# Optimization experiments

Hardware: AMD Instinct MI355X
Metric: run time of the kernel (lower is better)

Reference implementation:

```python
import jax, jax.numpy as jnp
import numpy as np

V, E, H, ENC_D, NL = 32000, 1024, 1024, 1024, 2
N, DEC_L, ENC_L, A = 32, 64, 64, 1024


def gru_cell(x, h, W_ih, W_hh, b_ih, b_hh):
    # PyTorch GRUCell math
    gi = x @ W_ih.T + b_ih            # N x 3H
    gh = h @ W_hh.T + b_hh            # N x 3H
    i_r, i_z, i_n = jnp.split(gi, 3, axis=-1)
    h_r, h_z, h_n = jnp.split(gh, 3, axis=-1)
    r = jax.nn.sigmoid(i_r + h_r)
    z = jax.nn.sigmoid(i_z + h_z)
    n = jnp.tanh(i_n + r * h_n)
    return (1.0 - z) * n + z * h


def setup_inputs() -> dict:
    key = jax.random.key(0)
    ks = jax.random.split(key, 16)
    s = 0.05
    emb_table = jax.random.normal(ks[0], (V, E), jnp.float32) * s
    emb_table = emb_table.at[0].set(0.0)  # padding_idx = 0
    inp = {
        "input_ids": jax.random.randint(ks[1], (N, DEC_L), 0, V),
        "dec_init": jax.random.normal(ks[2], (NL, N, H), jnp.float32),
        "enc_hids": jax.random.normal(ks[3], (N, ENC_L, ENC_D), jnp.float32),
        "emb_table": emb_table,
        "W_in": jax.random.normal(ks[4], (H, E), jnp.float32) * s,
        "b_in": jnp.zeros((H,), jnp.float32),
        "W_ctx": jax.random.normal(ks[5], (H, ENC_D), jnp.float32) * s,
        "b_ctx": jnp.zeros((H,), jnp.float32),
        "W_att_dec": jax.random.normal(ks[6], (A, H), jnp.float32) * s,
        "W_att_enc": jax.random.normal(ks[7], (A, ENC_D), jnp.float32) * s,
        "v_att": jax.random.normal(ks[8], (A,), jnp.float32) * s,
        "W_ih": jax.random.normal(ks[9], (NL, 3 * H, H), jnp.float32) * s,
        "W_hh": jax.random.normal(ks[10], (NL, 3 * H, H), jnp.float32) * s,
        "b_ih": jnp.zeros((NL, 3 * H), jnp.float32),
        "b_hh": jnp.zeros((NL, 3 * H), jnp.float32),
    }
    return inp


def reference(input_ids, dec_init, enc_hids, emb_table, W_in, b_in, W_ctx, b_ctx,
              W_att_dec, W_att_enc, v_att, W_ih, W_hh, b_ih, b_hh):
    ids = input_ids[:, :-1]                      # N x T (T = dec_L - 1)
    # precompute encoder side of additive attention: N x enc_L x A
    enc_proj = jnp.einsum('nld,ad->nla', enc_hids, W_att_enc)
    n_layers = W_ih.shape[0]

    def step(h_stack, x_ids):
        h_top = h_stack[-1]                       # N x H
        emb = emb_table[x_ids]                    # N x E
        # Bahdanau additive attention: v^T tanh(Wd h + We enc)
        dec_proj = h_top @ W_att_dec.T            # N x A
        score = jnp.einsum('nla,a->nl', jnp.tanh(enc_proj + dec_proj[:, None, :]), v_att)
        att = jax.nn.softmax(score, axis=-1)      # N x enc_L
        ctx = jnp.einsum('nl,nld->nd', att, enc_hids)  # N x enc_D
        merged = emb @ W_in.T + b_in + ctx @ W_ctx.T + b_ctx  # N x H
        layer_in = merged
        hs = []
        for l in range(n_layers):
            h_new = gru_cell(layer_in, h_stack[l], W_ih[l], W_hh[l], b_ih[l], b_hh[l])
            layer_in = h_new
            hs.append(h_new)
        new_stack = jnp.stack(hs, axis=0)
        return new_stack, (layer_in, att)

    dec_prev, (hs, atts) = jax.lax.scan(step, dec_init, ids.T)  # hs: T x N x H
    dec_hids = jnp.transpose(hs, (1, 0, 2))       # N x T x H
    atts = jnp.transpose(atts, (1, 2, 0))         # N x enc_L x T
    return dec_hids, atts, dec_prev
```

## Files before the change

### kernel.cpp

```cpp
#include <hip/hip_runtime.h>
#include <cstddef>

typedef unsigned short ushort_t;
typedef __attribute__((ext_vector_type(8))) short bhalf8;
typedef __attribute__((ext_vector_type(4))) unsigned short ushort4v;
typedef __attribute__((ext_vector_type(4))) float floatx4;

#define T_STEPS 63

__device__ __forceinline__ float bf2f(unsigned short u) {
  union { unsigned int i; float f; } c; c.i = ((unsigned int)u) << 16; return c.f;
}
__device__ __forceinline__ unsigned short f2bf(float f) {
  union { float f; unsigned int i; } c; c.f = f;
  unsigned int x = c.i;
  return (unsigned short)((x + 0x7FFFu + ((x >> 16) & 1u)) >> 16);
}
__device__ __forceinline__ float tanh_f(float x) {
  float e = exp2f(x * 2.8853900817779268f);
  return 1.f - 2.f / (e + 1.f);
}
__device__ __forceinline__ float sigm_f(float x) {
  return 1.f / (1.f + exp2f(x * -1.4426950408889634f));
}

__global__ __launch_bounds__(256) void conv_k(const float* __restrict__ in,
                                              ushort_t* __restrict__ outp, int n4) {
  int g = blockIdx.x * 256 + threadIdx.x;
  if (g < n4) {
    floatx4 v = ((const floatx4*)in)[g];
    ushort4v o;
    o[0] = f2bf(v[0]); o[1] = f2bf(v[1]); o[2] = f2bf(v[2]); o[3] = f2bf(v[3]);
    ((ushort4v*)outp)[g] = o;
  }
}

__global__ __launch_bounds__(256) void bsum_k(const float* __restrict__ b_in,
    const float* __restrict__ b_ctx, const float* __restrict__ v_att,
    float* __restrict__ bsum, ushort_t* __restrict__ vattbf) {
  int i = blockIdx.x * 256 + threadIdx.x;
  if (i < 1024) {
    bsum[i] = b_in[i] + b_ctx[i];
    vattbf[i] = f2bf(v_att[i]);
  }
}

__global__ __launch_bounds__(256) void init_k(const float* __restrict__ dec_init,
    float* __restrict__ h1, float* __restrict__ h2,
    ushort_t* __restrict__ h1bf, ushort_t* __restrict__ h2bf) {
  int g = blockIdx.x * 256 + threadIdx.x;
  int l = g >> 15, idx = g & 32767;
  float f = dec_init[g];
  if (l == 0) { h1[idx] = f; h1bf[idx] = f2bf(f); }
  else        { h2[idx] = f; h2bf[idx] = f2bf(f); }
}

__global__ __launch_bounds__(256) void encp_s(const float* __restrict__ enc_hids,
    const float* __restrict__ Wae, ushort_t* __restrict__ encp) {
  int g = blockIdx.x * 256 + threadIdx.x;
  int r = g >> 10, c = g & 1023;
  const float* x = enc_hids + (size_t)r * 1024;
  const float* w = Wae + (size_t)c * 1024;
  float s = 0.f;
  for (int k = 0; k < 1024; k += 4) {
    floatx4 a = *(const floatx4*)(x + k);
    floatx4 b = *(const floatx4*)(w + k);
    s += a[0] * b[0] + a[1] * b[1] + a[2] * b[2] + a[3] * b[3];
  }
  encp[g] = f2bf(s);
}

__global__ __launch_bounds__(256) void membp_s(const int* __restrict__ ids,
    const float* __restrict__ emb_table, const float* __restrict__ W_in,
    const float* __restrict__ bsum, ushort_t* __restrict__ membp) {
  int g = blockIdx.x * 256 + threadIdx.x;
  int row = g >> 10, c = g & 1023;
  int t = row >> 5, n = row & 31;
  const float* e = emb_table + (size_t)ids[n * 64 + t] * 1024;
  const float* w = W_in + (size_t)c * 1024;
  float s = bsum[c];
  for (int k = 0; k < 1024; k += 4) {
    floatx4 a = *(const floatx4*)(e + k);
    floatx4 b = *(const floatx4*)(w + k);
    s += a[0] * b[0] + a[1] * b[1] + a[2] * b[2] + a[3] * b[3];
  }
  membp[g] = f2bf(s);
}

__global__ __launch_bounds__(256) void stage0_k(
    const ushort_t* __restrict__ h1bf, const ushort_t* __restrict__ h2bf,
    const ushort_t* __restrict__ Wad, const ushort_t* __restrict__ Whh,
    const float* __restrict__ bhh,
    float* __restrict__ dprj, float* __restrict__ gh1, float* __restrict__ gh2) {
  __shared__ __align__(16) ushort_t sXk[32 * 264];
  __shared__ __align__(16) ushort_t sBk[32 * 264];
  int b = blockIdx.x, tid = threadIdx.x;
  int wid = tid >> 6, lane = tid & 63;
  int klane = (lane >> 4) << 3;
  const ushort_t *Xs, *Wp; const float* bp; float* Co; int ldc, colbase;
  if (b < 32)       { Xs = h2bf; Wp = Wad;           bp = nullptr;     Co = dprj; ldc = 1024; colbase = b * 32; }
  else if (b < 128) { Xs = h1bf; Wp = Whh;           bp = bhh;         Co = gh1;  ldc = 3072; colbase = (b - 32) * 32; }
  else              { Xs = h2bf; Wp = Whh + 3145728; bp = bhh + 3072;  Co = gh2;  ldc = 3072; colbase = (b - 128) * 32; }
  int nt = wid & 1, mt = wid >> 1;
  floatx4 acc = {0, 0, 0, 0};
  for (int kp = 0; kp < 4; ++kp) {
    __syncthreads();
    #pragma unroll
    for (int it = 0; it < 4; ++it) {
      int v = it * 256 + tid; int row = v >> 5, vc = v & 31;
      *(bhalf8*)(&sXk[row * 264 + vc * 8]) = *(const bhalf8*)(Xs + (size_t)row * 1024 + kp * 256 + vc * 8);
      *(bhalf8*)(&sBk[row * 264 + vc * 8]) = *(const bhalf8*)(Wp + (size_t)(colbase + row) * 1024 + kp * 256 + vc * 8);
    }
    __syncthreads();
    #pragma unroll
    for (int kit = 0; kit < 8; ++kit) {
      int k = kit * 32 + klane;
      bhalf8 a  = *(const bhalf8*)(&sXk[(mt * 16 + (lane & 15)) * 264 + k]);
      bhalf8 bf = *(const bhalf8*)(&sBk[(nt * 16 + (lane & 15)) * 264 + k]);
      acc = __builtin_amdgcn_mfma_f32_16x16x32_bf16(a, bf, acc, 0, 0, 0);
    }
  }
  int colw = colbase + nt * 16 + (lane & 15);
  float bv = bp ? bp[colw] : 0.f;
  int r0 = (lane >> 4) << 2;
  #pragma unroll
  for (int i = 0; i < 4; ++i)
    Co[(size_t)(mt * 16 + r0 + i) * ldc + colw] = acc[i] + bv;
}

__global__ __launch_bounds__(256) void att_k(int t,
    const ushort_t* __restrict__ encp, const float* __restrict__ dprj,
    const ushort_t* __restrict__ vattbf, const float* __restrict__ enc_hids,
    ushort_t* __restrict__ ctxbf, float* __restrict__ out_att) {
  __shared__ float sSc[64];
  __shared__ float sAtt[64];
  int n = blockIdx.x, tid = threadIdx.x;
  int l = tid >> 2, q = tid & 3;
  const ushort_t* ep = encp + ((size_t)(n * 64 + l)) * 1024 + q * 256;
  const float*    dp = dprj + n * 1024 + q * 256;
  float p = 0.f;
  for (int it = 0; it < 32; ++it) {
    bhalf8 E = *(const bhalf8*)(ep + it * 8);
    bhalf8 V = *(const bhalf8*)(vattbf + q * 256 + it * 8);
    #pragma unroll
    for (int r = 0; r < 8; ++r)
      p += tanh_f(bf2f((unsigned short)E[r]) + dp[it * 8 + r]) * bf2f((unsigned short)V[r]);
  }
  p += __shfl_down(p, 1, 4);
  p += __shfl_down(p, 2, 4);
  if (q == 0) sSc[l] = p;
  __syncthreads();
  if (tid < 64) {
    float s = sSc[tid];
    float m = s;
    for (int off = 32; off; off >>= 1) m = fmaxf(m, __shfl_xor(m, off));
    float e = exp2f((s - m) * 1.4426950408889634f);
    float sum = e;
    for (int off = 32; off; off >>= 1) sum += __shfl_xor(sum, off);
    float a = e / sum;
    sAtt[tid] = a;
    out_att[(size_t)n * 4032 + tid * 63 + t] = a;
  }
  __syncthreads();
  const float* er = enc_hids + ((size_t)n * 64) * 1024 + tid * 4;
  float c0 = 0, c1 = 0, c2 = 0, c3 = 0;
  for (int l2 = 0; l2 < 64; ++l2) {
    floatx4 ev = *(const floatx4*)(er + (size_t)l2 * 1024);
    float a = sAtt[l2];
    c0 += a * ev[0]; c1 += a * ev[1]; c2 += a * ev[2]; c3 += a * ev[3];
  }
  ushort_t* cp = ctxbf + n * 1024 + tid * 4;
  cp[0] = f2bf(c0); cp[1] = f2bf(c1); cp[2] = f2bf(c2); cp[3] = f2bf(c3);
}

__global__ __launch_bounds__(256) void mctx_k(
    const ushort_t* __restrict__ ctxbf, const ushort_t* __restrict__ Wctx,
    const ushort_t* __restrict__ membp_t, ushort_t* __restrict__ mctx) {
  __shared__ __align__(16) ushort_t sXk[32 * 264];
  __shared__ __align__(16) ushort_t sBk[32 * 264];
  int b = blockIdx.x, tid = threadIdx.x;
  int wid = tid >> 6, lane = tid & 63;
  int klane = (lane >> 4) << 3;
  int colbase = b * 32;
  int nt = wid & 1, mt = wid >> 1;
  floatx4 acc = {0, 0, 0, 0};
  for (int kp = 0; kp < 4; ++kp) {
    __syncthreads();
    #pragma unroll
    for (int it = 0; it < 4; ++it) {
      int v = it * 256 + tid; int row = v >> 5, vc = v & 31;
      *(bhalf8*)(&sXk[row * 264 + vc * 8]) = *(const bhalf8*)(ctxbf + (size_t)row * 1024 + kp * 256 + vc * 8);
      *(bhalf8*)(&sBk[row * 264 + vc * 8]) = *(const bhalf8*)(Wctx + (size_t)(colbase + row) * 1024 + kp * 256 + vc * 8);
    }
    __syncthreads();
    #pragma unroll
    for (int kit = 0; kit < 8; ++kit) {
      int k = kit * 32 + klane;
      bhalf8 a  = *(const bhalf8*)(&sXk[(mt * 16 + (lane & 15)) * 264 + k]);
      bhalf8 bf = *(const bhalf8*)(&sBk[(nt * 16 + (lane & 15)) * 264 + k]);
      acc = __builtin_amdgcn_mfma_f32_16x16x32_bf16(a, bf, acc, 0, 0, 0);
    }
  }
  int colw = colbase + nt * 16 + (lane & 15);
  int r0 = (lane >> 4) << 2;
  #pragma unroll
  for (int i = 0; i < 4; ++i) {
    int row = mt * 16 + r0 + i;
    mctx[(size_t)row * 1024 + colw] = f2bf(acc[i] + bf2f(membp_t[(size_t)row * 1024 + colw]));
  }
}

__global__ __launch_bounds__(256) void gru_k(
    const ushort_t* __restrict__ Xs, const ushort_t* __restrict__ Wg,
    const float* __restrict__ gh, const float* __restrict__ hp,
    float* __restrict__ ho, ushort_t* __restrict__ hobf,
    const float* __restrict__ add,
    float* __restrict__ outh) {
  __shared__ __align__(16) ushort_t sX16[16 * 1032];
  __shared__ __align__(16) float sRed[2304];
  int b = blockIdx.x, tid = threadIdx.x;
  int wid = tid >> 6, lane = tid & 63;
  int mh = b & 1, g = b >> 1, j0 = g * 16;
  #pragma unroll
  for (int it = 0; it < 8; ++it) {
    int v = it * 256 + tid; int row = v >> 7, vc = v & 127;
    *(bhalf8*)(&sX16[row * 1032 + vc * 8]) = *(const bhalf8*)(Xs + (size_t)(mh * 16 + row) * 1024 + vc * 8);
  }
  __syncthreads();
  floatx4 a0 = {0,0,0,0}, a1 = {0,0,0,0}, a2 = {0,0,0,0};
  int klane = (lane >> 4) << 3;
  const ushort_t* Wr = Wg + (size_t)(j0 + (lane & 15)) * 1024;
  for (int kit = 0; kit < 8; ++kit) {
    int k = wid * 256 + kit * 32 + klane;
    bhalf8 a = *(const bhalf8*)(&sX16[(lane & 15) * 1032 + k]);
    a0 = __builtin_amdgcn_mfma_f32_16x16x32_bf16(a, *(const bhalf8*)(Wr + k), a0, 0, 0, 0);
    a1 = __builtin_amdgcn_mfma_f32_16x16x32_bf16(a, *(const bhalf8*)(Wr + 1048576 + k), a1, 0, 0, 0);
    a2 = __builtin_amdgcn_mfma_f32_16x16x32_bf16(a, *(const bhalf8*)(Wr + 2097152 + k), a2, 0, 0, 0);
  }
  if (wid) {
    ((floatx4*)sRed)[((wid - 1) * 3 + 0) * 64 + lane] = a0;
    ((floatx4*)sRed)[((wid - 1) * 3 + 1) * 64 + lane] = a1;
    ((floatx4*)sRed)[((wid - 1) * 3 + 2) * 64 + lane] = a2;
  }
  __syncthreads();
  if (wid == 0) {
    #pragma unroll
    for (int w = 0; w < 3; ++w) {
      a0 += ((floatx4*)sRed)[(w * 3 + 0) * 64 + lane];
      a1 += ((floatx4*)sRed)[(w * 3 + 1) * 64 + lane];
      a2 += ((floatx4*)sRed)[(w * 3 + 2) * 64 + lane];
    }
    int col = j0 + (lane & 15), r0 = (lane >> 4) << 2;
    #pragma unroll
    for (int i = 0; i < 4; ++i) {
      int n = mh * 16 + r0 + i;
      float ir  = a0[i] + add[col];
      float iz  = a1[i] + add[col + 1024];
      float inn = a2[i] + add[col + 2048];
      int gb = n * 3072 + col;
      float r = sigm_f(ir + gh[gb]);
      float z = sigm_f(iz + gh[gb + 1024]);
      float nn = tanh_f(inn + r * gh[gb + 2048]);
      float h = (1.f - z) * nn + z * hp[n * 1024 + col];
      ho[n * 1024 + col] = h;
      hobf[n * 1024 + col] = f2bf(h);
      if (outh) outh[(size_t)n * 64512 + col] = h;
    }
  }
}

__global__ __launch_bounds__(256) void final_k(const float* __restrict__ h1,
                                               const float* __restrict__ h2,
                                               float* __restrict__ outp) {
  int b = blockIdx.x; int l = b >> 5, n = b & 31;
  const float* src = l ? h2 : h1;
  float* dst = outp + (size_t)l * 32768 + n * 1024;
  for (int c = threadIdx.x; c < 1024; c += 256) dst[c] = src[n * 1024 + c];
}

extern "C" void kernel_launch(void* const* d_in, const int* in_sizes, int n_in,
                              void* d_out, int out_size, void* d_ws, size_t ws_size,
                              hipStream_t stream) {
  const int*   input_ids = (const int*)d_in[0];
  const float* dec_init  = (const float*)d_in[1];
  const float* enc_hids  = (const float*)d_in[2];
  const float* emb_table = (const float*)d_in[3];
  const float* W_in      = (const float*)d_in[4];
  const float* b_in      = (const float*)d_in[5];
  const float* b_ctx     = (const float*)d_in[7];
  const float* W_att_dec = (const float*)d_in[8];
  const float* W_att_enc = (const float*)d_in[9];
  const float* v_att     = (const float*)d_in[10];
  const float* W_ih      = (const float*)d_in[11];
  const float* W_hh      = (const float*)d_in[12];
  const float* b_ih      = (const float*)d_in[13];
  const float* b_hh      = (const float*)d_in[14];
  const float* W_ctx     = (const float*)d_in[6];
  (void)in_sizes; (void)n_in; (void)out_size;

  const size_t WS_NEEDED = 39133184;
  if (ws_size < WS_NEEDED) return;
  char* ws = (char*)d_ws;
  float*    h1      = (float*)   (ws + 0);
  float*    h2      = (float*)   (ws + 131072);
  ushort_t* h1bf    = (ushort_t*)(ws + 262144);
  ushort_t* h2bf    = (ushort_t*)(ws + 327680);
  ushort_t* ctxbf   = (ushort_t*)(ws + 393216);
  ushort_t* mctx    = (ushort_t*)(ws + 458752);
  float*    dprj    = (float*)   (ws + 524288);
  float*    gh1     = (float*)   (ws + 655360);
  float*    gh2     = (float*)   (ws + 1048576);
  float*    bsum    = (float*)   (ws + 1441792);
  ushort_t* vattbf  = (ushort_t*)(ws + 1445888);
  ushort_t* encp    = (ushort_t*)(ws + 1449984);
  ushort_t* membp   = (ushort_t*)(ws + 5644288);
  ushort_t* Whh_bf  = (ushort_t*)(ws + 9773056);
  ushort_t* Wih_bf  = (ushort_t*)(ws + 22355968);
  ushort_t* Wad_bf  = (ushort_t*)(ws + 34938880);
  ushort_t* Wctx_bf = (ushort_t*)(ws + 37036032);

  float* out_hid  = (float*)d_out;
  float* out_att  = out_hid + 2064384;
  float* out_prev = out_att + 129024;

  bsum_k<<<dim3(4), dim3(256), 0, stream>>>(b_in, b_ctx, v_att, bsum, vattbf);
  init_k<<<dim3(256), dim3(256), 0, stream>>>(dec_init, h1, h2, h1bf, h2bf);
  conv_k<<<dim3(6144), dim3(256), 0, stream>>>(W_hh, Whh_bf, 1572864);
  conv_k<<<dim3(6144), dim3(256), 0, stream>>>(W_ih, Wih_bf, 1572864);
  conv_k<<<dim3(1024), dim3(256), 0, stream>>>(W_att_dec, Wad_bf, 262144);
  conv_k<<<dim3(1024), dim3(256), 0, stream>>>(W_ctx, Wctx_bf, 262144);
  encp_s<<<dim3(8192), dim3(256), 0, stream>>>(enc_hids, W_att_enc, encp);
  membp_s<<<dim3(8064), dim3(256), 0, stream>>>(input_ids, emb_table, W_in, bsum, membp);

  for (int t = 0; t < T_STEPS; ++t) {
    stage0_k<<<dim3(224), dim3(256), 0, stream>>>(h1bf, h2bf, Wad_bf, Whh_bf, b_hh,
                                                  dprj, gh1, gh2);
    att_k<<<dim3(32), dim3(256), 0, stream>>>(t, encp, dprj, vattbf, enc_hids,
                                              ctxbf, out_att);
    mctx_k<<<dim3(32), dim3(256), 0, stream>>>(ctxbf, Wctx_bf, membp + (size_t)t * 32768, mctx);
    gru_k<<<dim3(128), dim3(256), 0, stream>>>(mctx, Wih_bf, gh1, h1, h1, h1bf,
                                               b_ih, (float*)nullptr);
    gru_k<<<dim3(128), dim3(256), 0, stream>>>(h1bf, Wih_bf + 3145728, gh2, h2, h2, h2bf,
                                               b_ih + 3072, out_hid + (size_t)t * 1024);
  }
  final_k<<<dim3(64), dim3(256), 0, stream>>>(h1, h2, out_prev);
}
```

Baseline: 5.831 ms.

## Fuse decoder time loop into persistent kernel with global barriers

Replaces the per-step sequence of five kernel launches with one persistent 224-block kernel. Stages inside each step are separated by atomic-counter grid barriers, and the attention-to-merge dependency uses a smaller barrier over 32 blocks. The precomputed embedding projection (membp) is removed and computed per step inside the merge GEMM from gathered embedding rows and a bf16 W_in. The layer-1 Whh GEMM for the next step now overlaps the layer-2 GRU on idle blocks. This removes launch overhead but assumes all 224 blocks are co-resident, and the spin barrier has a bail-out that could silently break ordering.

```diff
diff --git a/kernel.cpp b/kernel.cpp
--- a/kernel.cpp
+++ b/kernel.cpp
@@ -7,6 +7,7 @@
 typedef __attribute__((ext_vector_type(4))) float floatx4;
 
 #define T_STEPS 63
+#define GRID_N 224
 
 __device__ __forceinline__ float bf2f(unsigned short u) {
   union { unsigned int i; float f; } c; c.i = ((unsigned int)u) << 16; return c.f;
@@ -37,8 +38,10 @@
 
 __global__ __launch_bounds__(256) void bsum_k(const float* __restrict__ b_in,
     const float* __restrict__ b_ctx, const float* __restrict__ v_att,
-    float* __restrict__ bsum, ushort_t* __restrict__ vattbf) {
+    float* __restrict__ bsum, ushort_t* __restrict__ vattbf,
+    unsigned* __restrict__ bar) {
   int i = blockIdx.x * 256 + threadIdx.x;
+  if (i == 0) { bar[0] = 0u; bar[128] = 0u; }
   if (i < 1024) {
     bsum[i] = b_in[i] + b_ctx[i];
     vattbf[i] = f2bf(v_att[i]);
@@ -70,37 +73,12 @@
   encp[g] = f2bf(s);
 }
 
-__global__ __launch_bounds__(256) void membp_s(const int* __restrict__ ids,
-    const float* __restrict__ emb_table, const float* __restrict__ W_in,
-    const float* __restrict__ bsum, ushort_t* __restrict__ membp) {
-  int g = blockIdx.x * 256 + threadIdx.x;
-  int row = g >> 10, c = g & 1023;
-  int t = row >> 5, n = row & 31;
-  const float* e = emb_table + (size_t)ids[n * 64 + t] * 1024;
-  const float* w = W_in + (size_t)c * 1024;
-  float s = bsum[c];
-  for (int k = 0; k < 1024; k += 4) {
-    floatx4 a = *(const floatx4*)(e + k);
-    floatx4 b = *(const floatx4*)(w + k);
-    s += a[0] * b[0] + a[1] * b[1] + a[2] * b[2] + a[3] * b[3];
-  }
-  membp[g] = f2bf(s);
-}
-
-__global__ __launch_bounds__(256) void stage0_k(
-    const ushort_t* __restrict__ h1bf, const ushort_t* __restrict__ h2bf,
-    const ushort_t* __restrict__ Wad, const ushort_t* __restrict__ Whh,
-    const float* __restrict__ bhh,
-    float* __restrict__ dprj, float* __restrict__ gh1, float* __restrict__ gh2) {
-  __shared__ __align__(16) ushort_t sXk[32 * 264];
-  __shared__ __align__(16) ushort_t sBk[32 * 264];
-  int b = blockIdx.x, tid = threadIdx.x;
+__device__ __forceinline__ void tile32(const ushort_t* __restrict__ Xs,
+    const ushort_t* __restrict__ Wp, const float* __restrict__ bias,
+    float* __restrict__ Co, int ldc, int colbase,
+    ushort_t* sXk, ushort_t* sBk, int tid) {
   int wid = tid >> 6, lane = tid & 63;
   int klane = (lane >> 4) << 3;
-  const ushort_t *Xs, *Wp; const float* bp; float* Co; int ldc, colbase;
-  if (b < 32)       { Xs = h2bf; Wp = Wad;           bp = nullptr;     Co = dprj; ldc = 1024; colbase = b * 32; }
-  else if (b < 128) { Xs = h1bf; Wp = Whh;           bp = bhh;         Co = gh1;  ldc = 3072; colbase = (b - 32) * 32; }
-  else              { Xs = h2bf; Wp = Whh + 3145728; bp = bhh + 3072;  Co = gh2;  ldc = 3072; colbase = (b - 128) * 32; }
   int nt = wid & 1, mt = wid >> 1;
   floatx4 acc = {0, 0, 0, 0};
   for (int kp = 0; kp < 4; ++kp) {
@@ -121,104 +99,55 @@
     }
   }
   int colw = colbase + nt * 16 + (lane & 15);
-  float bv = bp ? bp[colw] : 0.f;
+  float bv = bias ? bias[colw] : 0.f;
   int r0 = (lane >> 4) << 2;
   #pragma unroll
   for (int i = 0; i < 4; ++i)
     Co[(size_t)(mt * 16 + r0 + i) * ldc + colw] = acc[i] + bv;
 }
 
-__global__ __launch_bounds__(256) void att_k(int t,
-    const ushort_t* __restrict__ encp, const float* __restrict__ dprj,
-    const ushort_t* __restrict__ vattbf, const float* __restrict__ enc_hids,
-    ushort_t* __restrict__ ctxbf, float* __restrict__ out_att) {
-  __shared__ float sSc[64];
-  __shared__ float sAtt[64];
-  int n = blockIdx.x, tid = threadIdx.x;
-  int l = tid >> 2, q = tid & 3;
-  const ushort_t* ep = encp + ((size_t)(n * 64 + l)) * 1024 + q * 256;
-  const float*    dp = dprj + n * 1024 + q * 256;
-  float p = 0.f;
-  for (int it = 0; it < 32; ++it) {
-    bhalf8 E = *(const bhalf8*)(ep + it * 8);
-    bhalf8 V = *(const bhalf8*)(vattbf + q * 256 + it * 8);
-    #pragma unroll
-    for (int r = 0; r < 8; ++r)
-      p += tanh_f(bf2f((unsigned short)E[r]) + dp[it * 8 + r]) * bf2f((unsigned short)V[r]);
-  }
-  p += __shfl_down(p, 1, 4);
-  p += __shfl_down(p, 2, 4);
-  if (q == 0) sSc[l] = p;
-  __syncthreads();
-  if (tid < 64) {
-    float s = sSc[tid];
-    float m = s;
-    for (int off = 32; off; off >>= 1) m = fmaxf(m, __shfl_xor(m, off));
-    float e = exp2f((s - m) * 1.4426950408889634f);
-    float sum = e;
-    for (int off = 32; off; off >>= 1) sum += __shfl_xor(sum, off);
-    float a = e / sum;
-    sAtt[tid] = a;
-    out_att[(size_t)n * 4032 + tid * 63 + t] = a;
-  }
-  __syncthreads();
-  const float* er = enc_hids + ((size_t)n * 64) * 1024 + tid * 4;
-  float c0 = 0, c1 = 0, c2 = 0, c3 = 0;
-  for (int l2 = 0; l2 < 64; ++l2) {
-    floatx4 ev = *(const floatx4*)(er + (size_t)l2 * 1024);
-    float a = sAtt[l2];
-    c0 += a * ev[0]; c1 += a * ev[1]; c2 += a * ev[2]; c3 += a * ev[3];
-  }
-  ushort_t* cp = ctxbf + n * 1024 + tid * 4;
-  cp[0] = f2bf(c0); cp[1] = f2bf(c1); cp[2] = f2bf(c2); cp[3] = f2bf(c3);
-}
-
-__global__ __launch_bounds__(256) void mctx_k(
-    const ushort_t* __restrict__ ctxbf, const ushort_t* __restrict__ Wctx,
-    const ushort_t* __restrict__ membp_t, ushort_t* __restrict__ mctx) {
+__global__ __launch_bounds__(256) void ginit_k(const ushort_t* __restrict__ h1bf,
+    const ushort_t* __restrict__ Whh, const float* __restrict__ bhh,
+    float* __restrict__ gh1) {
   __shared__ __align__(16) ushort_t sXk[32 * 264];
   __shared__ __align__(16) ushort_t sBk[32 * 264];
-  int b = blockIdx.x, tid = threadIdx.x;
-  int wid = tid >> 6, lane = tid & 63;
-  int klane = (lane >> 4) << 3;
-  int colbase = b * 32;
-  int nt = wid & 1, mt = wid >> 1;
-  floatx4 acc = {0, 0, 0, 0};
-  for (int kp = 0; kp < 4; ++kp) {
-    __syncthreads();
-    #pragma unroll
-    for (int it = 0; it < 4; ++it) {
-      int v = it * 256 + tid; int row = v >> 5, vc = v & 31;
-      *(bhalf8*)(&sXk[row * 264 + vc * 8]) = *(const bhalf8*)(ctxbf + (size_t)row * 1024 + kp * 256 + vc * 8);
-      *(bhalf8*)(&sBk[row * 264 + vc * 8]) = *(const bhalf8*)(Wctx + (size_t)(colbase + row) * 1024 + kp * 256 + vc * 8);
-    }
-    __syncthreads();
-    #pragma unroll
-    for (int kit = 0; kit < 8; ++kit) {
-      int k = kit * 32 + klane;
-      bhalf8 a  = *(const bhalf8*)(&sXk[(mt * 16 + (lane & 15)) * 264 + k]);
-      bhalf8 bf = *(const bhalf8*)(&sBk[(nt * 16 + (lane & 15)) * 264 + k]);
-      acc = __builtin_amdgcn_mfma_f32_16x16x32_bf16(a, bf, acc, 0, 0, 0);
-    }
-  }
-  int colw = colbase + nt * 16 + (lane & 15);
-  int r0 = (lane >> 4) << 2;
-  #pragma unroll
-  for (int i = 0; i < 4; ++i) {
-    int row = mt * 16 + r0 + i;
-    mctx[(size_t)row * 1024 + colw] = f2bf(acc[i] + bf2f(membp_t[(size_t)row * 1024 + colw]));
-  }
-}
-
-__global__ __launch_bounds__(256) void gru_k(
+  tile32(h1bf, Whh, bhh, gh1, 3072, blockIdx.x * 32, sXk, sBk, threadIdx.x);
+}
+
+struct PArgs {
+  const float *enc_hids, *bhh, *bih, *emb_table, *bsum;
+  const int* ids;
+  const ushort_t *Whh, *Wih, *Wad, *Wctx, *Win, *encp, *vatt;
+  float *h1, *h2, *dprj, *gh1, *gh2;
+  ushort_t *h1bf, *h2bf, *ctxbf, *mctxbf;
+  float *out_hid, *out_att, *out_prev;
+  unsigned* bar;
+};
+
+__device__ __forceinline__ void gbar_n(unsigned* bar, unsigned& ph, unsigned nblk) {
+  __syncthreads();
+  if (threadIdx.x == 0) {
+    __threadfence();
+    __hip_atomic_fetch_add(bar, 1u, __ATOMIC_RELAXED, __HIP_MEMORY_SCOPE_AGENT);
+    unsigned tgt = (++ph) * nblk;
+    unsigned spins = 0;
+    while (__hip_atomic_load(bar, __ATOMIC_RELAXED, __HIP_MEMORY_SCOPE_AGENT) < tgt) {
+      if (spins < 8)       __builtin_amdgcn_s_sleep(2);
+      else if (spins < 32) __builtin_amdgcn_s_sleep(16);
+      else                 __builtin_amdgcn_s_sleep(64);
+      if (++spins > (1u << 20)) break;
+    }
+    __threadfence();
+  }
+  __syncthreads();
+}
+
+__device__ __forceinline__ void gru_body(int b, int tid,
     const ushort_t* __restrict__ Xs, const ushort_t* __restrict__ Wg,
     const float* __restrict__ gh, const float* __restrict__ hp,
     float* __restrict__ ho, ushort_t* __restrict__ hobf,
-    const float* __restrict__ add,
-    float* __restrict__ outh) {
-  __shared__ __align__(16) ushort_t sX16[16 * 1032];
-  __shared__ __align__(16) float sRed[2304];
-  int b = blockIdx.x, tid = threadIdx.x;
+    const float* __restrict__ add, float* __restrict__ outh,
+    ushort_t* sX16, float* sRed) {
   int wid = tid >> 6, lane = tid & 63;
   int mh = b & 1, g = b >> 1, j0 = g * 16;
   #pragma unroll
@@ -269,13 +198,143 @@
   }
 }
 
-__global__ __launch_bounds__(256) void final_k(const float* __restrict__ h1,
-                                               const float* __restrict__ h2,
-                                               float* __restrict__ outp) {
-  int b = blockIdx.x; int l = b >> 5, n = b & 31;
-  const float* src = l ? h2 : h1;
-  float* dst = outp + (size_t)l * 32768 + n * 1024;
-  for (int c = threadIdx.x; c < 1024; c += 256) dst[c] = src[n * 1024 + c];
+__global__ __launch_bounds__(256) void decoder_pers(PArgs A) {
+  __shared__ __align__(16) unsigned char smemU[42240];
+  __shared__ float sSc[64];
+  __shared__ float sAtt[64];
+  __shared__ int sIds[32];
+  ushort_t* sXk  = (ushort_t*)smemU;
+  ushort_t* sBk  = (ushort_t*)(smemU + 16896);
+  ushort_t* sX16 = (ushort_t*)smemU;
+  float*    sRed = (float*)(smemU + 33024);
+
+  const int b = blockIdx.x, tid = threadIdx.x;
+  unsigned ph = 0, phm = 0;
+  unsigned* barF = A.bar;
+  unsigned* barM = A.bar + 128;
+
+  for (int t = 0; t < T_STEPS; ++t) {
+    if (b < 32)        tile32(A.h2bf, A.Wad, nullptr, A.dprj, 1024, b * 32, sXk, sBk, tid);
+    else if (b < 128)  tile32(A.h2bf, A.Whh + 3145728, A.bhh + 3072, A.gh2, 3072, (b - 32) * 32, sXk, sBk, tid);
+    gbar_n(barF, ph, GRID_N);
+
+    if (b < 32) {
+      int n = b;
+      int l = tid >> 2, q = tid & 3;
+      const ushort_t* ep = A.encp + ((size_t)(n * 64 + l)) * 1024 + q * 256;
+      const float*    dp = A.dprj + n * 1024 + q * 256;
+      float p = 0.f;
+      for (int it = 0; it < 32; ++it) {
+        bhalf8 E = *(const bhalf8*)(ep + it * 8);
+        bhalf8 V = *(const bhalf8*)(A.vatt + q * 256 + it * 8);
+        #pragma unroll
+        for (int r = 0; r < 8; ++r)
+          p += tanh_f(bf2f((unsigned short)E[r]) + dp[it * 8 + r]) * bf2f((unsigned short)V[r]);
+      }
+      p += __shfl_down(p, 1, 4);
+      p += __shfl_down(p, 2, 4);
+      if (q == 0) sSc[l] = p;
+      __syncthreads();
+      if (tid < 64) {
+        float s = sSc[tid];
+        float m = s;
+        for (int off = 32; off; off >>= 1) m = fmaxf(m, __shfl_xor(m, off));
+        float e = exp2f((s - m) * 1.4426950408889634f);
+        float sum = e;
+        for (int off = 32; off; off >>= 1) sum += __shfl_xor(sum, off);
+        float a = e / sum;
+        sAtt[tid] = a;
+        A.out_att[(size_t)n * 4032 + tid * 63 + t] = a;
+      }
+      __syncthreads();
+      const float* er = A.enc_hids + ((size_t)n * 64) * 1024 + tid * 4;
+      float c0 = 0, c1 = 0, c2 = 0, c3 = 0;
+      for (int l2 = 0; l2 < 64; ++l2) {
+        floatx4 ev = *(const floatx4*)(er + (size_t)l2 * 1024);
+        float a = sAtt[l2];
+        c0 += a * ev[0]; c1 += a * ev[1]; c2 += a * ev[2]; c3 += a * ev[3];
+      }
+      ushort_t* cp = A.ctxbf + n * 1024 + tid * 4;
+      cp[0] = f2bf(c0); cp[1] = f2bf(c1); cp[2] = f2bf(c2); cp[3] = f2bf(c3);
+
+      gbar_n(barM, phm, 32);
+
+      int colbase = b * 32;
+      if (tid < 32) sIds[tid] = A.ids[tid * 64 + t];
+      __syncthreads();
+      int wid = tid >> 6, lane = tid & 63;
+      int klane = (lane >> 4) << 3;
+      int nt = wid & 1, mt = wid >> 1;
+      floatx4 acc = {0, 0, 0, 0};
+      for (int kp = 0; kp < 4; ++kp) {
+        __syncthreads();
+        #pragma unroll
+        for (int it = 0; it < 4; ++it) {
+          int v = it * 256 + tid; int row = v >> 5, vc = v & 31;
+          *(bhalf8*)(&sXk[row * 264 + vc * 8]) = *(const bhalf8*)(A.ctxbf + (size_t)row * 1024 + kp * 256 + vc * 8);
+          *(bhalf8*)(&sBk[row * 264 + vc * 8]) = *(const bhalf8*)(A.Wctx + (size_t)(colbase + row) * 1024 + kp * 256 + vc * 8);
+        }
+        __syncthreads();
+        #pragma unroll
+        for (int kit = 0; kit < 8; ++kit) {
+          int k = kit * 32 + klane;
+          bhalf8 a  = *(const bhalf8*)(&sXk[(mt * 16 + (lane & 15)) * 264 + k]);
+          bhalf8 bf = *(const bhalf8*)(&sBk[(nt * 16 + (lane & 15)) * 264 + k]);
+          acc = __builtin_amdgcn_mfma_f32_16x16x32_bf16(a, bf, acc, 0, 0, 0);
+        }
+        __syncthreads();
+        #pragma unroll
+        for (int it = 0; it < 4; ++it) {
+          int v = it * 256 + tid; int row = v >> 5, vc = v & 31;
+          const float* epp = A.emb_table + (size_t)sIds[row] * 1024 + kp * 256 + vc * 8;
+          floatx4 f0 = *(const floatx4*)epp;
+          floatx4 f1 = *(const floatx4*)(epp + 4);
+          bhalf8 o;
+          o[0] = (short)f2bf(f0[0]); o[1] = (short)f2bf(f0[1]);
+          o[2] = (short)f2bf(f0[2]); o[3] = (short)f2bf(f0[3]);
+          o[4] = (short)f2bf(f1[0]); o[5] = (short)f2bf(f1[1]);
+          o[6] = (short)f2bf(f1[2]); o[7] = (short)f2bf(f1[3]);
+          *(bhalf8*)(&sXk[row * 264 + vc * 8]) = o;
+          *(bhalf8*)(&sBk[row * 264 + vc * 8]) = *(const bhalf8*)(A.Win + (size_t)(colbase + row) * 1024 + kp * 256 + vc * 8);
+        }
+        __syncthreads();
+        #pragma unroll
+        for (int kit = 0; kit < 8; ++kit) {
+          int k = kit * 32 + klane;
+          bhalf8 a  = *(const bhalf8*)(&sXk[(mt * 16 + (lane & 15)) * 264 + k]);
+          bhalf8 bf = *(const bhalf8*)(&sBk[(nt * 16 + (lane & 15)) * 264 + k]);
+          acc = __builtin_amdgcn_mfma_f32_16x16x32_bf16(a, bf, acc, 0, 0, 0);
+        }
+      }
+      int colw = colbase + nt * 16 + (lane & 15);
+      int r0 = (lane >> 4) << 2;
+      #pragma unroll
+      for (int i = 0; i < 4; ++i) {
+        int row = mt * 16 + r0 + i;
+        A.mctxbf[(size_t)row * 1024 + colw] = f2bf(acc[i] + A.bsum[colw]);
+      }
+    }
+    gbar_n(barF, ph, GRID_N);
+
+    if (b < 128)
+      gru_body(b, tid, A.mctxbf, A.Wih, A.gh1, A.h1, A.h1, A.h1bf,
+               A.bih, nullptr, sX16, sRed);
+    gbar_n(barF, ph, GRID_N);
+
+    if (b < 128)
+      gru_body(b, tid, A.h1bf, A.Wih + 3145728, A.gh2, A.h2, A.h2, A.h2bf,
+               A.bih + 3072, A.out_hid + (size_t)t * 1024, sX16, sRed);
+    else
+      tile32(A.h1bf, A.Whh, A.bhh, A.gh1, 3072, (b - 128) * 32, sXk, sBk, tid);
+    gbar_n(barF, ph, GRID_N);
+  }
+
+  if (b < 64) {
+    int l = b >> 5, n = b & 31;
+    const float* src = l ? A.h2 : A.h1;
+    float* dst = A.out_prev + (size_t)l * 32768 + n * 1024;
+    for (int c = tid; c < 1024; c += 256) dst[c] = src[n * 1024 + c];
+  }
 }
 
 extern "C" void kernel_launch(void* const* d_in, const int* in_sizes, int n_in,
@@ -287,6 +346,7 @@
   const float* emb_table = (const float*)d_in[3];
   const float* W_in      = (const float*)d_in[4];
   const float* b_in      = (const float*)d_in[5];
+  const float* W_ctx     = (const float*)d_in[6];
   const float* b_ctx     = (const float*)d_in[7];
   const float* W_att_dec = (const float*)d_in[8];
   const float* W_att_enc = (const float*)d_in[9];
@@ -295,10 +355,9 @@
   const float* W_hh      = (const float*)d_in[12];
   const float* b_ih      = (const float*)d_in[13];
   const float* b_hh      = (const float*)d_in[14];
-  const float* W_ctx     = (const float*)d_in[6];
   (void)in_sizes; (void)n_in; (void)out_size;
 
-  const size_t WS_NEEDED = 39133184;
+  const size_t WS_NEEDED = 37105664;
   if (ws_size < WS_NEEDED) return;
   char* ws = (char*)d_ws;
   float*    h1      = (float*)   (ws + 0);
@@ -306,42 +365,42 @@
   ushort_t* h1bf    = (ushort_t*)(ws + 262144);
   ushort_t* h2bf    = (ushort_t*)(ws + 327680);
   ushort_t* ctxbf   = (ushort_t*)(ws + 393216);
-  ushort_t* mctx    = (ushort_t*)(ws + 458752);
+  ushort_t* mctxbf  = (ushort_t*)(ws + 458752);
   float*    dprj    = (float*)   (ws + 524288);
   float*    gh1     = (float*)   (ws + 655360);
   float*    gh2     = (float*)   (ws + 1048576);
   float*    bsum    = (float*)   (ws + 1441792);
   ushort_t* vattbf  = (ushort_t*)(ws + 1445888);
-  ushort_t* encp    = (ushort_t*)(ws + 1449984);
-  ushort_t* membp   = (ushort_t*)(ws + 5644288);
-  ushort_t* Whh_bf  = (ushort_t*)(ws + 9773056);
-  ushort_t* Wih_bf  = (ushort_t*)(ws + 22355968);
-  ushort_t* Wad_bf  = (ushort_t*)(ws + 34938880);
-  ushort_t* Wctx_bf = (ushort_t*)(ws + 37036032);
+  unsigned* bar     = (unsigned*)(ws + 1449984);
+  ushort_t* encp    = (ushort_t*)(ws + 1454080);
+  ushort_t* Win_bf  = (ushort_t*)(ws + 5648384);
+  ushort_t* Wctx_bf = (ushort_t*)(ws + 7745536);
+  ushort_t* Wad_bf  = (ushort_t*)(ws + 9842688);
+  ushort_t* Whh_bf  = (ushort_t*)(ws + 11939840);
+  ushort_t* Wih_bf  = (ushort_t*)(ws + 24522752);
 
   float* out_hid  = (float*)d_out;
   float* out_att  = out_hid + 2064384;
   float* out_prev = out_att + 129024;
 
-  bsum_k<<<dim3(4), dim3(256), 0, stream>>>(b_in, b_ctx, v_att, bsum, vattbf);
+  bsum_k<<<dim3(4), dim3(256), 0, stream>>>(b_in, b_ctx, v_att, bsum, vattbf, bar);
   init_k<<<dim3(256), dim3(256), 0, stream>>>(dec_init, h1, h2, h1bf, h2bf);
   conv_k<<<dim3(6144), dim3(256), 0, stream>>>(W_hh, Whh_bf, 1572864);
   conv_k<<<dim3(6144), dim3(256), 0, stream>>>(W_ih, Wih_bf, 1572864);
   conv_k<<<dim3(1024), dim3(256), 0, stream>>>(W_att_dec, Wad_bf, 262144);
   conv_k<<<dim3(1024), dim3(256), 0, stream>>>(W_ctx, Wctx_bf, 262144);
+  conv_k<<<dim3(1024), dim3(256), 0, stream>>>(W_in, Win_bf, 262144);
   encp_s<<<dim3(8192), dim3(256), 0, stream>>>(enc_hids, W_att_enc, encp);
-  membp_s<<<dim3(8064), dim3(256), 0, stream>>>(input_ids, emb_table, W_in, bsum, membp);
-
-  for (int t = 0; t < T_STEPS; ++t) {
-    stage0_k<<<dim3(224), dim3(256), 0, stream>>>(h1bf, h2bf, Wad_bf, Whh_bf, b_hh,
-                                                  dprj, gh1, gh2);
-    att_k<<<dim3(32), dim3(256), 0, stream>>>(t, encp, dprj, vattbf, enc_hids,
-                                              ctxbf, out_att);
-    mctx_k<<<dim3(32), dim3(256), 0, stream>>>(ctxbf, Wctx_bf, membp + (size_t)t * 32768, mctx);
-    gru_k<<<dim3(128), dim3(256), 0, stream>>>(mctx, Wih_bf, gh1, h1, h1, h1bf,
-                                               b_ih, (float*)nullptr);
-    gru_k<<<dim3(128), dim3(256), 0, stream>>>(h1bf, Wih_bf + 3145728, gh2, h2, h2, h2bf,
-                                               b_ih + 3072, out_hid + (size_t)t * 1024);
-  }
-  final_k<<<dim3(64), dim3(256), 0, stream>>>(h1, h2, out_prev);
-}
+  ginit_k<<<dim3(96), dim3(256), 0, stream>>>(h1bf, Whh_bf, b_hh, gh1);
+
+  PArgs A;
+  A.enc_hids = enc_hids; A.bhh = b_hh; A.bih = b_ih; A.emb_table = emb_table;
+  A.bsum = bsum; A.ids = input_ids;
+  A.Whh = Whh_bf; A.Wih = Wih_bf; A.Wad = Wad_bf; A.Wctx = Wctx_bf; A.Win = Win_bf;
+  A.encp = encp; A.vatt = vattbf;
+  A.h1 = h1; A.h2 = h2; A.dprj = dprj; A.gh1 = gh1; A.gh2 = gh2;
+  A.h1bf = h1bf; A.h2bf = h2bf; A.ctxbf = ctxbf; A.mctxbf = mctxbf;
+  A.out_hid = out_hid; A.out_att = out_att; A.out_prev = out_prev;
+  A.bar = bar;
+  decoder_pers<<<dim3(GRID_N), dim3(256), 0, stream>>>(A);
+}
```

After: 11.86 ms. 2.03x slower.
